# Kernel tuning notes

Measured on AMD Instinct MI355X. Metric: run time of the kernel, lower is better.

Reference implementation:

```python
import jax, jax.numpy as jnp
import numpy as np

PH, PW = 7, 7          # pooled_height, pooled_width
SCALE = 0.0625         # spatial_scale
K = 6                  # static max integer cells per bin side (max bin size = 448*SCALE/7 = 4)


def setup_inputs() -> dict:
    key = jax.random.key(0)
    kf, kb, kx, ky, kw, kh = jax.random.split(key, 6)
    B, C, H, W = 4, 256, 64, 64
    R = 1024
    features = jax.random.normal(kf, (B, C, H, W), dtype=jnp.float32)
    # rois rows: (batch_idx, x1, y1, x2, y2) in image coords (image ~1024px, scale 1/16)
    bidx = jax.random.randint(kb, (R,), 0, B).astype(jnp.float32)
    x1 = jax.random.uniform(kx, (R,), minval=0.0, maxval=576.0)
    y1 = jax.random.uniform(ky, (R,), minval=0.0, maxval=576.0)
    bw = jax.random.uniform(kw, (R,), minval=32.0, maxval=448.0)
    bh = jax.random.uniform(kh, (R,), minval=32.0, maxval=448.0)
    rois = jnp.stack([bidx, x1, y1, x1 + bw, y1 + bh], axis=1)
    return {"features": features, "rois": rois}


def _gather(features, b, hidx, widx, H, W):
    # hidx: [R,PH] int32, widx: [R,PW] int32 -> [R,PH,PW,C]; out-of-bounds reads are zero
    vh = (hidx >= 0) & (hidx < H)
    vw = (widx >= 0) & (widx < W)
    mask = (vh[:, :, None] & vw[:, None, :]).astype(features.dtype)  # [R,PH,PW]
    hc = jnp.clip(hidx, 0, H - 1)
    wc = jnp.clip(widx, 0, W - 1)
    d = features[b[:, None, None], :, hc[:, :, None], wc[:, None, :]]  # [R,PH,PW,C]
    return d * mask[..., None]


def _cell_weights(start, end, s):
    # exact integrals of the two 1D bilinear hat weights over [start,end] clipped to cell [s, s+1]
    y0 = jnp.maximum(start, s)
    yl = jnp.maximum(jnp.minimum(end, s + 1.0), y0)  # empty intersection -> zero weights
    a = y0 - s
    la = yl - s
    g0 = la - 0.5 * la * la - a + 0.5 * a * a  # weight of node at s
    g1 = 0.5 * la * la - 0.5 * a * a           # weight of node at s+1
    return g0, g1


def prroi_pool(features, rois):
    B, C, H, W = features.shape
    R = rois.shape[0]
    dt = features.dtype
    b = rois[:, 0].astype(jnp.int32)
    x1 = rois[:, 1] * SCALE
    y1 = rois[:, 2] * SCALE
    x2 = rois[:, 3] * SCALE
    y2 = rois[:, 4] * SCALE
    roi_w = jnp.maximum(x2 - x1, 0.0)
    roi_h = jnp.maximum(y2 - y1, 0.0)
    bin_w = roi_w / PW
    bin_h = roi_h / PH
    # per-bin continuous windows [ws, we)
    ws_w = x1[:, None] + bin_w[:, None] * jnp.arange(PW, dtype=dt)  # [R,PW]
    ws_h = y1[:, None] + bin_h[:, None] * jnp.arange(PH, dtype=dt)  # [R,PH]
    we_w = ws_w + bin_w[:, None]
    we_h = ws_h + bin_h[:, None]
    s0_w = jnp.floor(ws_w)
    s0_h = jnp.floor(ws_h)

    offs = np.stack(np.meshgrid(np.arange(K), np.arange(K), indexing="ij"), -1).reshape(-1, 2)
    offs = jnp.asarray(offs, dtype=dt)  # [K*K, 2] (dh, dw)

    def step(acc, off):
        sh = s0_h + off[0]  # [R,PH] float (integer-valued)
        sw = s0_w + off[1]  # [R,PW]
        gy0, gy1 = _cell_weights(ws_h, we_h, sh)
        gx0, gx1 = _cell_weights(ws_w, we_w, sw)
        hi = sh.astype(jnp.int32)
        wi = sw.astype(jnp.int32)
        d00 = _gather(features, b, hi, wi, H, W)
        d01 = _gather(features, b, hi, wi + 1, H, W)
        d10 = _gather(features, b, hi + 1, wi, H, W)
        d11 = _gather(features, b, hi + 1, wi + 1, H, W)
        gy0 = gy0[:, :, None, None]
        gy1 = gy1[:, :, None, None]
        gx0 = gx0[:, None, :, None]
        gx1 = gx1[:, None, :, None]
        contrib = d00 * (gy0 * gx0) + d01 * (gy0 * gx1) + d10 * (gy1 * gx0) + d11 * (gy1 * gx1)
        return acc + contrib, None

    acc0 = jnp.zeros((R, PH, PW, C), dtype=dt)
    acc, _ = jax.lax.scan(step, acc0, offs)
    win = (bin_w * bin_h)[:, None, None, None]  # bin area in feature coords
    out = jnp.where(win > 0, acc / jnp.where(win > 0, win, 1.0), 0.0)
    return jnp.transpose(out, (0, 3, 1, 2))  # [R, C, PH, PW]


def reference(features, rois):
    return prroi_pool(features, rois)
```

## Files before the change

kernel.cpp:

```cpp
#include <hip/hip_runtime.h>
#include <hip/hip_fp16.h>

#define R_    1024
#define B_    4
#define C_    256
#define H_    64
#define W_    64
#define HW_   4096
#define PHW_  49
#define ROIT  128
#define LROWF 258
#define SLACKH 17408

__device__ __forceinline__ void cell_w(float start, float end, float s, float& g0, float& g1) {
    float y0 = fmaxf(start, s);
    float yl = fmaxf(fminf(end, s + 1.0f), y0);
    float a  = y0 - s;
    float la = yl - s;
    g0 = la - 0.5f * la * la - a + 0.5f * a * a;
    g1 = 0.5f * la * la - 0.5f * a * a;
}

__device__ __forceinline__ float4 h4_to_f4(uint2 u) {
    __half2 a = *reinterpret_cast<__half2*>(&u.x);
    __half2 b = *reinterpret_cast<__half2*>(&u.y);
    float2 fa = __half22float2(a);
    float2 fb = __half22float2(b);
    return make_float4(fa.x, fa.y, fb.x, fb.y);
}

__global__ __launch_bounds__(256) void prep(const float* __restrict__ in,
                                            __half* __restrict__ fTh,
                                            const float* __restrict__ rois,
                                            int* __restrict__ perm,
                                            float* __restrict__ roitab) {
    int bid = blockIdx.x;
    if (bid < 4096) {
        __shared__ float tile[32][33];
        int b   = bid >> 10;
        int rem = bid & 1023;
        int c0  = (rem >> 7) * 32;
        int p0  = (rem & 127) * 32;
        int tx  = threadIdx.x & 31;
        int ty  = threadIdx.x >> 5;
        const float* src = in + (size_t)b * C_ * HW_;
#pragma unroll
        for (int i = 0; i < 32; i += 8)
            tile[ty + i][tx] = src[(size_t)(c0 + ty + i) * HW_ + (p0 + tx)];
        __syncthreads();
        __half2* dsth = (__half2*)(fTh + (size_t)b * HW_ * C_);
#pragma unroll
        for (int i = 0; i < 2; ++i) {
            int idx = threadIdx.x + i * 256;
            int py  = idx >> 4;
            int cp  = idx & 15;
            float lo = tile[cp * 2][py];
            float hi = tile[cp * 2 + 1][py];
            dsth[(size_t)(p0 + py) * (C_ / 2) + (c0 >> 1) + cp] = __floats2half2_rn(lo, hi);
        }
        return;
    }
    if (bid == 4096) {
        if (threadIdx.x >= 64) {
            for (int j = threadIdx.x - 64; j < SLACKH; j += 192)
                fTh[(size_t)B_ * HW_ * C_ + j] = __half(0.0f);
            return;
        }
        int lane = threadIdx.x;
        unsigned long long below = (1ull << lane) - 1ull;
        int key[16];
#pragma unroll
        for (int i = 0; i < 16; ++i) {
            int idx = i * 64 + lane;
            const float* roi = rois + idx * 5;
            int b = (int)roi[0];
            float yc = (roi[2] + roi[4]) * 0.5f * 0.0625f;
            int yb = min(3, max(0, (int)(yc * 0.0625f)));
            key[i] = b * 4 + yb;
        }
        int cntk[16];
#pragma unroll
        for (int k = 0; k < 16; ++k) cntk[k] = 0;
        for (int i = 0; i < 16; ++i)
#pragma unroll
            for (int k = 0; k < 16; ++k)
                cntk[k] += __popcll(__ballot(key[i] == k));
        int off[16]; int acc = 0;
#pragma unroll
        for (int k = 0; k < 16; ++k) { off[k] = acc; acc += cntk[k]; }
        for (int i = 0; i < 16; ++i) {
#pragma unroll
            for (int k = 0; k < 16; ++k) {
                unsigned long long m = __ballot(key[i] == k);
                if (key[i] == k)
                    perm[off[k] + __popcll(m & below)] = i * 64 + lane;
                off[k] += __popcll(m);
            }
        }
        return;
    }
    int i = (bid - 4097) * 256 + threadIdx.x;
    int r  = i / PHW_;
    int k  = i - r * PHW_;
    int ph = k / 7, pw = k - ph * 7;
    const float* roi = rois + r * 5;
    int bb = (int)roi[0];
    float x1 = roi[1] * 0.0625f, y1 = roi[2] * 0.0625f;
    float x2 = roi[3] * 0.0625f, y2 = roi[4] * 0.0625f;
    float rw = fmaxf(x2 - x1, 0.0f), rh = fmaxf(y2 - y1, 0.0f);
    float bw = rw / 7.0f, bh = rh / 7.0f;
    float win = bw * bh;
    float* rt = roitab + (size_t)r * ROIT;

    float wy[8], wx[7];
#pragma unroll
    for (int t = 0; t < 7; ++t) { wy[t] = 0.0f; wx[t] = 0.0f; }
    wy[7] = 0.0f;
    int w0 = 0, h0 = 0, npy = 0, w00 = 0;
    float invwin = 0.0f;
    if (win > 0.0f) {
        float ws = x1 + bw * (float)pw, we = ws + bw;
        float hs = y1 + bh * (float)ph, he = hs + bh;
        float s0w = floorf(ws), s0h = floorf(hs);
        w0 = (int)s0w; h0 = (int)s0h;
        w00 = (int)floorf(x1);
#pragma unroll
        for (int o = 0; o < 6; ++o) {
            float g0, g1;
            cell_w(hs, he, s0h + (float)o, g0, g1);
            wy[o] += g0; wy[o + 1] += g1;
            cell_w(ws, we, s0w + (float)o, g0, g1);
            wx[o] += g0; wx[o + 1] += g1;
        }
        npy = min(7, max(0, (int)ceilf(he - s0h + 1.0f)));
        int npx = min(7, max(0, (int)ceilf(we - s0w + 1.0f)));
        npy = max(0, min(npy, H_ - h0));
        npx = max(0, min(npx, W_ - w0));
#pragma unroll
        for (int t = 0; t < 7; ++t) {
            if (t >= npx) wx[t] = 0.0f;
            if (t >= npy) wy[t] = 0.0f;
        }
        invwin = 1.0f / win;
    }
    if (ph == 0) {
#pragma unroll
        for (int t = 0; t < 7; ++t) rt[pw * 7 + t] = wx[t];
        rt[49 + pw] = __int_as_float(w0 - w00);
    }
    if (pw == 0) {
#pragma unroll
        for (int t = 0; t < 8; ++t) rt[72 + ph * 8 + t] = wy[t] * invwin;
        rt[64 + ph] = __int_as_float(h0 | (npy << 8));
    }
    if (k == 0) {
        int jlim = 0;
        if (win > 0.0f) {
#pragma unroll
            for (int p = 0; p < 7; ++p) {
                float wsp = x1 + bw * (float)p, wep = wsp + bw;
                float s0wp = floorf(wsp);
                int w0p = (int)s0wp;
                int npxp = min(7, max(0, (int)ceilf(wep - s0wp + 1.0f)));
                npxp = max(0, min(npxp, W_ - w0p));
                jlim = max(jlim, (w0p - w00) + npxp);
            }
        }
        rt[63] = __int_as_float(bb | (w00 << 8) | (jlim << 16));
    }
}

__global__ __launch_bounds__(256, 8) void prroi_rows(const __half* __restrict__ fTh,
                                                     const int* __restrict__ perm,
                                                     const float* __restrict__ roitab,
                                                     __half* __restrict__ scr) {
    __shared__ __align__(16) float colw[4][32 * 8];
    int wid  = __builtin_amdgcn_readfirstlane(threadIdx.x >> 6);
    int lane = threadIdx.x & 63;
    float* cwv = colw[wid];
    int bid = blockIdx.x;
    int xcd = bid & 7;
    int s   = (bid >> 3) * 4 + wid;
    if (s >= 896) return;
    int t   = (s & 31) * 28 + (s >> 5);
    int g   = xcd * 896 + t;
    int rs  = g / 7;
    int ph  = g - rs * 7;
    int r   = __builtin_amdgcn_readfirstlane(perm[rs]);
    const float* rt = roitab + (size_t)r * ROIT;

#pragma unroll
    for (int u = 0; u < 4; ++u) cwv[lane + u * 64] = 0.0f;
    if (lane < 49) {
        int pw = lane / 7;
        int dx = lane - pw * 7;
        float wxv = rt[lane];
        int d = __float_as_int(rt[49 + pw]);
        cwv[(d + dx) * 8 + pw] = wxv;
    }
    int meta = __float_as_int(rt[63]);
    int bb   = meta & 0xff;
    int w00  = (meta >> 8) & 0xff;
    int jlim = (meta >> 16) & 0xff;
    int hm   = __float_as_int(rt[64 + ph]);
    int h0   = hm & 0xff;
    int npy  = (hm >> 8) & 0xff;
    int npy2 = (npy + 1) & ~1;
    const float* wyp = rt + 72 + ph * 8;
    const __half* fr = fTh + ((size_t)bb * HW_ + (size_t)h0 * W_ + w00) * C_ + lane * 4;

    float4 acc[7];
#pragma unroll
    for (int p = 0; p < 7; ++p) acc[p] = make_float4(0.f, 0.f, 0.f, 0.f);

    for (int jl = 0; jl < jlim; jl += 2) {
        const __half* cp = fr + (size_t)jl * C_;
        float4 gA = make_float4(0.f, 0.f, 0.f, 0.f);
        float4 gB = make_float4(0.f, 0.f, 0.f, 0.f);
        for (int dy = 0; dy < npy2; dy += 2) {
            const __half* r0 = cp + (size_t)dy * (W_ * C_);
            uint2 va0 = *(const uint2*)(r0);
            uint2 vb0 = *(const uint2*)(r0 + C_);
            uint2 va1 = *(const uint2*)(r0 + W_ * C_);
            uint2 vb1 = *(const uint2*)(r0 + W_ * C_ + C_);
            float w0y = wyp[dy];
            float w1y = wyp[dy + 1];
            float4 fa0 = h4_to_f4(va0);
            float4 fb0 = h4_to_f4(vb0);
            float4 fa1 = h4_to_f4(va1);
            float4 fb1 = h4_to_f4(vb1);
            gA.x = fmaf(w0y, fa0.x, fmaf(w1y, fa1.x, gA.x));
            gA.y = fmaf(w0y, fa0.y, fmaf(w1y, fa1.y, gA.y));
            gA.z = fmaf(w0y, fa0.z, fmaf(w1y, fa1.z, gA.z));
            gA.w = fmaf(w0y, fa0.w, fmaf(w1y, fa1.w, gA.w));
            gB.x = fmaf(w0y, fb0.x, fmaf(w1y, fb1.x, gB.x));
            gB.y = fmaf(w0y, fb0.y, fmaf(w1y, fb1.y, gB.y));
            gB.z = fmaf(w0y, fb0.z, fmaf(w1y, fb1.z, gB.z));
            gB.w = fmaf(w0y, fb0.w, fmaf(w1y, fb1.w, gB.w));
        }
        float4 ca0 = *(const float4*)(cwv + jl * 8);
        float4 ca1 = *(const float4*)(cwv + jl * 8 + 4);
        float4 cb0 = *(const float4*)(cwv + jl * 8 + 8);
        float4 cb1 = *(const float4*)(cwv + jl * 8 + 12);
#define ACCP(P, CA, CB) { \
    acc[P].x = fmaf(CA, gA.x, fmaf(CB, gB.x, acc[P].x)); \
    acc[P].y = fmaf(CA, gA.y, fmaf(CB, gB.y, acc[P].y)); \
    acc[P].z = fmaf(CA, gA.z, fmaf(CB, gB.z, acc[P].z)); \
    acc[P].w = fmaf(CA, gA.w, fmaf(CB, gB.w, acc[P].w)); }
        ACCP(0, ca0.x, cb0.x); ACCP(1, ca0.y, cb0.y); ACCP(2, ca0.z, cb0.z);
        ACCP(3, ca0.w, cb0.w); ACCP(4, ca1.x, cb1.x); ACCP(5, ca1.y, cb1.y);
        ACCP(6, ca1.z, cb1.z);
#undef ACCP
    }
    __half* sb = scr + ((size_t)r * PHW_ + ph * 7) * C_ + lane * 4;
#pragma unroll
    for (int p = 0; p < 7; ++p) {
        union { __half2 h2[2]; uint2 u; } pk2;
        pk2.h2[0] = __floats2half2_rn(acc[p].x, acc[p].y);
        pk2.h2[1] = __floats2half2_rn(acc[p].z, acc[p].w);
        *(uint2*)(sb + (size_t)p * C_) = pk2.u;
    }
}

__global__ __launch_bounds__(256) void fixup(const int* __restrict__ perm,
                                             const __half* __restrict__ scr,
                                             float* __restrict__ out) {
    __shared__ __align__(4) __half lds_h[PHW_ * LROWF];
    int bid  = blockIdx.x;
    int spos = ((bid & 7) << 7) | (bid >> 3);
    int r    = perm[spos];
    const unsigned int* src = (const unsigned int*)(scr + (size_t)r * PHW_ * C_);
    for (int j = threadIdx.x; j < PHW_ * (C_ / 2); j += 256) {
        int row = j >> 7;
        int col = j & 127;
        *(unsigned int*)&lds_h[row * LROWF + col * 2] = src[j];
    }
    __syncthreads();
    float* outr = out + (size_t)r * (C_ * PHW_);
#pragma unroll 4
    for (int j = threadIdx.x; j < C_ * PHW_; j += 256) {
        int c = j / PHW_;
        int k = j - c * PHW_;
        outr[j] = __half2float(lds_h[k * LROWF + c]);
    }
}

__global__ __launch_bounds__(256) void prroi_pool_direct(const float* __restrict__ f,
                                                         const float* __restrict__ rois,
                                                         float* __restrict__ out) {
    int bin = blockIdx.x;
    int r  = bin / PHW_;
    int k  = bin - r * PHW_;
    int ph = k / 7;
    int pw = k - ph * 7;
    int c = threadIdx.x;

    const float* roi = rois + r * 5;
    int bb = (int)roi[0];
    float x1 = roi[1] * 0.0625f, y1 = roi[2] * 0.0625f;
    float x2 = roi[3] * 0.0625f, y2 = roi[4] * 0.0625f;
    float rw = fmaxf(x2 - x1, 0.0f), rh = fmaxf(y2 - y1, 0.0f);
    float bw = rw / 7.0f, bh = rh / 7.0f;
    float win = bw * bh;
    size_t oidx = ((size_t)r * C_ + c) * PHW_ + k;
    if (!(win > 0.0f)) { out[oidx] = 0.0f; return; }

    float ws = x1 + bw * (float)pw, we = ws + bw;
    float hs = y1 + bh * (float)ph, he = hs + bh;
    float s0w = floorf(ws), s0h = floorf(hs);
    int w0 = (int)s0w, h0 = (int)s0h;
    float wy[7], wx[7];
#pragma unroll
    for (int t = 0; t < 7; ++t) { wy[t] = 0.0f; wx[t] = 0.0f; }
#pragma unroll
    for (int o = 0; o < 6; ++o) {
        float g0, g1;
        cell_w(hs, he, s0h + (float)o, g0, g1);
        wy[o] += g0; wy[o + 1] += g1;
        cell_w(ws, we, s0w + (float)o, g0, g1);
        wx[o] += g0; wx[o + 1] += g1;
    }
    int npy = min(7, max(0, (int)ceilf(he - s0h + 1.0f)));
    int npx = min(7, max(0, (int)ceilf(we - s0w + 1.0f)));
    npy = max(0, min(npy, H_ - h0));
    npx = max(0, min(npx, W_ - w0));

    const float* fbc = f + ((size_t)bb * C_ + c) * (H_ * W_);
    float acc = 0.0f;
#pragma unroll
    for (int dy = 0; dy < 7; ++dy) {
        if (dy < npy) {
            float row = 0.0f;
#pragma unroll
            for (int dx = 0; dx < 7; ++dx) {
                if (dx < npx)
                    row = fmaf(wx[dx], fbc[(h0 + dy) * W_ + (w0 + dx)], row);
            }
            acc = fmaf(wy[dy], row, acc);
        }
    }
    out[oidx] = acc / win;
}

extern "C" void kernel_launch(void* const* d_in, const int* in_sizes, int n_in,
                              void* d_out, int out_size, void* d_ws, size_t ws_size,
                              hipStream_t stream) {
    const float* feat = (const float*)d_in[0];
    const float* rois = (const float*)d_in[1];
    float* out = (float*)d_out;

    const size_t fth_b   = (size_t)B_ * HW_ * C_ * sizeof(__half);
    const size_t slack_b = (size_t)SLACKH * sizeof(__half);
    const size_t perm_b  = (size_t)R_ * sizeof(int);
    const size_t rt_b    = (size_t)R_ * ROIT * sizeof(float);
    const size_t scr_b   = (size_t)R_ * PHW_ * C_ * sizeof(__half);

    const size_t base = fth_b + slack_b + perm_b + rt_b;
    if (ws_size >= base + scr_b) {
        __half* fTh  = (__half*)d_ws;
        int*    perm = (int*)((char*)d_ws + fth_b + slack_b);
        float*  rtab = (float*)((char*)d_ws + fth_b + slack_b + perm_b);
        __half* scr  = (__half*)((char*)d_ws + base);
        prep<<<4293, 256, 0, stream>>>(feat, fTh, rois, perm, rtab);
        prroi_rows<<<2048, 256, 0, stream>>>(fTh, perm, rtab, scr);
        fixup<<<R_, 256, 0, stream>>>(perm, scr, out);
    } else {
        prroi_pool_direct<<<R_ * PHW_, 256, 0, stream>>>(feat, rois, out);
    }
}
```

Before: 65.81 us.

## Split wavefront across column pairs with 16-byte loads and shuffle reduction

The rows kernel now has each half of the wavefront handle one column of every column pair, with each lane covering 8 channels through 16-byte loads in place of 8-byte ones. The two halves' partial sums are combined with a cross-half shuffle, and the stores are split so each half writes a different subset of the 7 outputs. The goal is wider memory transactions and fewer load instructions. In exchange, accumulator registers double to 56 floats and the occupancy hint in launch bounds is dropped, which may lower occupancy.

```diff
diff --git a/kernel.cpp b/kernel.cpp
--- a/kernel.cpp
+++ b/kernel.cpp
@@ -21,12 +21,15 @@
     g1 = 0.5f * la * la - 0.5f * a * a;
 }
 
-__device__ __forceinline__ float4 h4_to_f4(uint2 u) {
-    __half2 a = *reinterpret_cast<__half2*>(&u.x);
-    __half2 b = *reinterpret_cast<__half2*>(&u.y);
-    float2 fa = __half22float2(a);
-    float2 fb = __half22float2(b);
-    return make_float4(fa.x, fa.y, fb.x, fb.y);
+__device__ __forceinline__ void h8_fma(uint4 v, float w, float4& ga, float4& gb) {
+    __half2 h0 = *(__half2*)&v.x, h1 = *(__half2*)&v.y;
+    __half2 h2 = *(__half2*)&v.z, h3 = *(__half2*)&v.w;
+    float2 f0 = __half22float2(h0), f1 = __half22float2(h1);
+    float2 f2 = __half22float2(h2), f3 = __half22float2(h3);
+    ga.x = fmaf(w, f0.x, ga.x); ga.y = fmaf(w, f0.y, ga.y);
+    ga.z = fmaf(w, f1.x, ga.z); ga.w = fmaf(w, f1.y, ga.w);
+    gb.x = fmaf(w, f2.x, gb.x); gb.y = fmaf(w, f2.y, gb.y);
+    gb.z = fmaf(w, f3.x, gb.z); gb.w = fmaf(w, f3.y, gb.w);
 }
 
 __global__ __launch_bounds__(256) void prep(const float* __restrict__ in,
@@ -170,10 +173,10 @@
     }
 }
 
-__global__ __launch_bounds__(256, 8) void prroi_rows(const __half* __restrict__ fTh,
-                                                     const int* __restrict__ perm,
-                                                     const float* __restrict__ roitab,
-                                                     __half* __restrict__ scr) {
+__global__ __launch_bounds__(256) void prroi_rows(const __half* __restrict__ fTh,
+                                                  const int* __restrict__ perm,
+                                                  const float* __restrict__ roitab,
+                                                  __half* __restrict__ scr) {
     __shared__ __align__(16) float colw[4][32 * 8];
     int wid  = __builtin_amdgcn_readfirstlane(threadIdx.x >> 6);
     int lane = threadIdx.x & 63;
@@ -207,58 +210,71 @@
     int npy  = (hm >> 8) & 0xff;
     int npy2 = (npy + 1) & ~1;
     const float* wyp = rt + 72 + ph * 8;
-    const __half* fr = fTh + ((size_t)bb * HW_ + (size_t)h0 * W_ + w00) * C_ + lane * 4;
-
-    float4 acc[7];
-#pragma unroll
-    for (int p = 0; p < 7; ++p) acc[p] = make_float4(0.f, 0.f, 0.f, 0.f);
+
+    int half = lane >> 5;
+    int cl   = lane & 31;
+    const __half* fr = fTh + ((size_t)bb * HW_ + (size_t)h0 * W_ + w00 + half) * C_ + cl * 8;
+
+    float4 aA[7], aB[7];
+#pragma unroll
+    for (int p = 0; p < 7; ++p) {
+        aA[p] = make_float4(0.f, 0.f, 0.f, 0.f);
+        aB[p] = make_float4(0.f, 0.f, 0.f, 0.f);
+    }
 
     for (int jl = 0; jl < jlim; jl += 2) {
+        const float* cw = cwv + (jl + half) * 8;
+        float4 c0 = *(const float4*)(cw);
+        float4 c1 = *(const float4*)(cw + 4);
         const __half* cp = fr + (size_t)jl * C_;
         float4 gA = make_float4(0.f, 0.f, 0.f, 0.f);
         float4 gB = make_float4(0.f, 0.f, 0.f, 0.f);
         for (int dy = 0; dy < npy2; dy += 2) {
             const __half* r0 = cp + (size_t)dy * (W_ * C_);
-            uint2 va0 = *(const uint2*)(r0);
-            uint2 vb0 = *(const uint2*)(r0 + C_);
-            uint2 va1 = *(const uint2*)(r0 + W_ * C_);
-            uint2 vb1 = *(const uint2*)(r0 + W_ * C_ + C_);
+            uint4 va = *(const uint4*)(r0);
+            uint4 vb = *(const uint4*)(r0 + W_ * C_);
             float w0y = wyp[dy];
             float w1y = wyp[dy + 1];
-            float4 fa0 = h4_to_f4(va0);
-            float4 fb0 = h4_to_f4(vb0);
-            float4 fa1 = h4_to_f4(va1);
-            float4 fb1 = h4_to_f4(vb1);
-            gA.x = fmaf(w0y, fa0.x, fmaf(w1y, fa1.x, gA.x));
-            gA.y = fmaf(w0y, fa0.y, fmaf(w1y, fa1.y, gA.y));
-            gA.z = fmaf(w0y, fa0.z, fmaf(w1y, fa1.z, gA.z));
-            gA.w = fmaf(w0y, fa0.w, fmaf(w1y, fa1.w, gA.w));
-            gB.x = fmaf(w0y, fb0.x, fmaf(w1y, fb1.x, gB.x));
-            gB.y = fmaf(w0y, fb0.y, fmaf(w1y, fb1.y, gB.y));
-            gB.z = fmaf(w0y, fb0.z, fmaf(w1y, fb1.z, gB.z));
-            gB.w = fmaf(w0y, fb0.w, fmaf(w1y, fb1.w, gB.w));
-        }
-        float4 ca0 = *(const float4*)(cwv + jl * 8);
-        float4 ca1 = *(const float4*)(cwv + jl * 8 + 4);
-        float4 cb0 = *(const float4*)(cwv + jl * 8 + 8);
-        float4 cb1 = *(const float4*)(cwv + jl * 8 + 12);
-#define ACCP(P, CA, CB) { \
-    acc[P].x = fmaf(CA, gA.x, fmaf(CB, gB.x, acc[P].x)); \
-    acc[P].y = fmaf(CA, gA.y, fmaf(CB, gB.y, acc[P].y)); \
-    acc[P].z = fmaf(CA, gA.z, fmaf(CB, gB.z, acc[P].z)); \
-    acc[P].w = fmaf(CA, gA.w, fmaf(CB, gB.w, acc[P].w)); }
-        ACCP(0, ca0.x, cb0.x); ACCP(1, ca0.y, cb0.y); ACCP(2, ca0.z, cb0.z);
-        ACCP(3, ca0.w, cb0.w); ACCP(4, ca1.x, cb1.x); ACCP(5, ca1.y, cb1.y);
-        ACCP(6, ca1.z, cb1.z);
-#undef ACCP
-    }
-    __half* sb = scr + ((size_t)r * PHW_ + ph * 7) * C_ + lane * 4;
+            h8_fma(va, w0y, gA, gB);
+            h8_fma(vb, w1y, gA, gB);
+        }
+#define APPLY(P, CP) { \
+    aA[P].x = fmaf(CP, gA.x, aA[P].x); aA[P].y = fmaf(CP, gA.y, aA[P].y); \
+    aA[P].z = fmaf(CP, gA.z, aA[P].z); aA[P].w = fmaf(CP, gA.w, aA[P].w); \
+    aB[P].x = fmaf(CP, gB.x, aB[P].x); aB[P].y = fmaf(CP, gB.y, aB[P].y); \
+    aB[P].z = fmaf(CP, gB.z, aB[P].z); aB[P].w = fmaf(CP, gB.w, aB[P].w); }
+        APPLY(0, c0.x); APPLY(1, c0.y); APPLY(2, c0.z); APPLY(3, c0.w);
+        APPLY(4, c1.x); APPLY(5, c1.y); APPLY(6, c1.z);
+#undef APPLY
+    }
+
 #pragma unroll
     for (int p = 0; p < 7; ++p) {
-        union { __half2 h2[2]; uint2 u; } pk2;
-        pk2.h2[0] = __floats2half2_rn(acc[p].x, acc[p].y);
-        pk2.h2[1] = __floats2half2_rn(acc[p].z, acc[p].w);
-        *(uint2*)(sb + (size_t)p * C_) = pk2.u;
+        aA[p].x += __shfl_xor(aA[p].x, 32);
+        aA[p].y += __shfl_xor(aA[p].y, 32);
+        aA[p].z += __shfl_xor(aA[p].z, 32);
+        aA[p].w += __shfl_xor(aA[p].w, 32);
+        aB[p].x += __shfl_xor(aB[p].x, 32);
+        aB[p].y += __shfl_xor(aB[p].y, 32);
+        aB[p].z += __shfl_xor(aB[p].z, 32);
+        aB[p].w += __shfl_xor(aB[p].w, 32);
+    }
+
+    __half* sb = scr + ((size_t)r * PHW_ + ph * 7) * C_ + cl * 8;
+#pragma unroll
+    for (int s4 = 0; s4 < 4; ++s4) {
+        const int ihi = (4 + s4 > 6) ? 6 : 4 + s4;
+        float4 pa = half ? aA[ihi] : aA[s4];
+        float4 pb = half ? aB[ihi] : aB[s4];
+        int p = half ? 4 + s4 : s4;
+        if (p < 7) {
+            union { __half2 h2[4]; uint4 u; } pk;
+            pk.h2[0] = __floats2half2_rn(pa.x, pa.y);
+            pk.h2[1] = __floats2half2_rn(pa.z, pa.w);
+            pk.h2[2] = __floats2half2_rn(pb.x, pb.y);
+            pk.h2[3] = __floats2half2_rn(pb.z, pb.w);
+            *(uint4*)(sb + (size_t)p * C_) = pk.u;
+        }
     }
 }
 
```

Measured after the change: 63.38 us. 3.7% less time.
